# Kernel tuning notes

Hardware: AMD Instinct MI355X
Metric: run time of the kernel (lower is better)

The kernel has to match this reference:

```python
import jax, jax.numpy as jnp
from jax import lax
import numpy as np

B = 512
EPS = 1e-5


def _conv(x, w, b):
    # x: [B,C,H,W], w: [O,I,3,3], stride 1, pad 1 (same spatial)
    y = lax.conv_general_dilated(x, w, window_strides=(1, 1),
                                 padding=[(1, 1), (1, 1)],
                                 dimension_numbers=('NCHW', 'OIHW', 'NCHW'))
    return y + b[None, :, None, None]


def _bn(x, g, b, m, v):
    # eval-mode batchnorm with running stats
    inv = g * lax.rsqrt(v + EPS)
    return x * inv[None, :, None, None] + (b - m * inv)[None, :, None, None]


def _maxpool2(x):
    return lax.reduce_window(x, -jnp.inf, lax.max, (1, 1, 2, 2), (1, 1, 2, 2), 'VALID')


def _block(x, w, b, g, be, m, v):
    return _maxpool2(jax.nn.relu(_bn(_conv(x, w, b), g, be, m, v)))


def setup_inputs() -> dict:
    key = jax.random.key(0)
    ks = jax.random.split(key, 12)
    n = lambda k, s: jax.random.normal(k, s, jnp.float32) * 0.05
    z = lambda s: jnp.zeros(s, jnp.float32)
    o = lambda s: jnp.ones(s, jnp.float32)
    return {
        'x': jax.random.normal(ks[0], (B, 1, 48, 48), jnp.float32),
        'conv1_w': n(ks[1], (256, 1, 3, 3)), 'conv1_b': z((256,)),
        'bn1_g': o((256,)), 'bn1_b': z((256,)), 'bn1_m': z((256,)), 'bn1_v': o((256,)),
        'conv2_w': n(ks[2], (128, 256, 3, 3)), 'conv2_b': z((128,)),
        'bn2_g': o((128,)), 'bn2_b': z((128,)), 'bn2_m': z((128,)), 'bn2_v': o((128,)),
        'conv3_w': n(ks[3], (64, 128, 3, 3)), 'conv3_b': z((64,)),
        'bn3_g': o((64,)), 'bn3_b': z((64,)), 'bn3_m': z((64,)), 'bn3_v': o((64,)),
        'fc1_w': n(ks[4], (512, 2304)), 'fc1_b': z((512,)),
        'fc2_w': n(ks[5], (256, 512)), 'fc2_b': z((256,)),
        'att_w': n(ks[6], (64, 256)), 'att_b': z((64,)),
        'fc3_w': n(ks[7], (7, 64)), 'fc3_b': z((7,)),
    }


def reference(x, conv1_w, conv1_b, bn1_g, bn1_b, bn1_m, bn1_v,
              conv2_w, conv2_b, bn2_g, bn2_b, bn2_m, bn2_v,
              conv3_w, conv3_b, bn3_g, bn3_b, bn3_m, bn3_v,
              fc1_w, fc1_b, fc2_w, fc2_b, att_w, att_b, fc3_w, fc3_b):
    out1 = _block(x, conv1_w, conv1_b, bn1_g, bn1_b, bn1_m, bn1_v)      # [B,256,24,24]
    out2 = _block(out1, conv2_w, conv2_b, bn2_g, bn2_b, bn2_m, bn2_v)   # [B,128,12,12]
    out3 = _block(out2, conv3_w, conv3_b, bn3_g, bn3_b, bn3_m, bn3_v)   # [B,64,6,6]
    b_ = out3.shape[0]
    out4 = out3.reshape(b_, -1)                                          # [B,2304]
    out5 = out4 @ fc1_w.T + fc1_b                                        # [B,512]
    out6 = out5 @ fc2_w.T + fc2_b                                        # [B,256]
    # spatial attention: query projected to channel dim of out3
    q = out6 @ att_w.T + att_b                                           # [B,64]
    scores = jnp.einsum('bchw,bc->bhw', out3, q).reshape(b_, -1)         # [B,36]
    attn = jax.nn.softmax(scores, axis=1).reshape(b_, 6, 6)
    g_mod = jnp.einsum('bchw,bhw->bc', out3, attn)                       # [B,64]
    return g_mod @ fc3_w.T + fc3_b                                       # [B,7]
```

## Files before the change

### kernel.cpp

```cpp
#include <hip/hip_runtime.h>
#include <hip/hip_bf16.h>
#include <math.h>

#define EPS_BN 1e-5f

typedef __bf16 bf16x8 __attribute__((ext_vector_type(8)));
typedef float f32x4 __attribute__((ext_vector_type(4)));
typedef float f32x2 __attribute__((ext_vector_type(2)));

__device__ __forceinline__ void gl2lds16(const void* g, void* l) {
  __builtin_amdgcn_global_load_lds(
      (const __attribute__((address_space(1))) unsigned int*)g,
      (__attribute__((address_space(3))) unsigned int*)l, 16, 0, 0);
}

__global__ __launch_bounds__(256) void k_conv1(
    const float* __restrict__ x, const float* __restrict__ w,
    const float* __restrict__ cb, const float* __restrict__ g,
    const float* __restrict__ bb, const float* __restrict__ m,
    const float* __restrict__ v, __hip_bfloat16* __restrict__ out1p,
    __hip_bfloat16* __restrict__ out2p, const float* __restrict__ W32,
    const float* __restrict__ fc1w, float* __restrict__ Wet, int n1) {
  __shared__ float xp[14 * 50];
  const int bq = blockIdx.x;
  const int t = threadIdx.x;
  if (bq >= n1) {
    int idx = (bq - n1) * 256 + t;
    int r = idx / 2304, c = idx - r * 2304;
    float s = 0.f;
    for (int k = 0; k < 512; k++)
      s = fmaf(W32[r * 512 + k], fc1w[k * 2304 + c], s);
    Wet[c * 64 + r] = s;
    return;
  }
  const int b = bq >> 2, q = bq & 3;
  __hip_bfloat16* ob = out1p + (size_t)b * (26 * 26 * 256);
  const __hip_bfloat16 z = __float2bfloat16(0.f);
  if (q == 0)
    for (int i = t; i < 26 * 256; i += 256) ob[i] = z;
  if (q == 3)
    for (int i = t; i < 26 * 256; i += 256) ob[25 * 26 * 256 + i] = z;
  for (int i = t; i < 6 * 2 * 256; i += 256) {
    int r = 1 + 6 * q + (i >> 9), side = (i >> 8) & 1, c = i & 255;
    ob[(r * 26 + side * 25) * 256 + c] = z;
  }
  {
    __hip_bfloat16* o2 = out2p + (size_t)b * (14 * 14 * 128);
    if (q == 0)
      for (int i = t; i < 14 * 128; i += 256) o2[i] = z;
    if (q == 1)
      for (int i = t; i < 14 * 128; i += 256) o2[13 * 14 * 128 + i] = z;
    if (q == 2)
      for (int i = t; i < 6 * 2 * 128; i += 256) {
        int r = 1 + (i >> 8), side = (i >> 7) & 1, c = i & 127;
        o2[(r * 14 + side * 13) * 128 + c] = z;
      }
    if (q == 3)
      for (int i = t; i < 6 * 2 * 128; i += 256) {
        int r = 7 + (i >> 8), side = (i >> 7) & 1, c = i & 127;
        o2[(r * 14 + side * 13) * 128 + c] = z;
      }
  }
  for (int i = t; i < 14 * 50; i += 256) xp[i] = 0.f;
  __syncthreads();
  const float* xb = x + (size_t)b * 2304;
  for (int i = t; i < 14 * 48; i += 256) {
    int rr = i / 48, c = i - rr * 48;
    int gr = 12 * q - 1 + rr;
    if (gr >= 0 && gr < 48) xp[rr * 50 + c + 1] = xb[gr * 48 + c];
  }
  __syncthreads();
  float wr[9];
#pragma unroll
  for (int i = 0; i < 9; i++) wr[i] = w[t * 9 + i];
  const float scale = g[t] * rsqrtf(v[t] + EPS_BN);
  const float bias = (cb[t] - m[t]) * scale + bb[t];
#pragma unroll
  for (int ohl = 0; ohl < 6; ohl++) {
    const int r0 = 2 * ohl;
    f32x2 c01[4];
#pragma unroll
    for (int r = 0; r < 4; r++) c01[r] = *(const f32x2*)&xp[(r0 + r) * 50];
#pragma unroll 4
    for (int ow = 0; ow < 24; ow++) {
      f32x2 c23[4];
#pragma unroll
      for (int r = 0; r < 4; r++)
        c23[r] = *(const f32x2*)&xp[(r0 + r) * 50 + 2 * ow + 2];
      f32x2 s2a = 0.f, s2b = 0.f;
#pragma unroll
      for (int r = 0; r < 4; r++) {
        f32x2 p0 = c01[r], p2 = c23[r];
        f32x2 p1 = {p0.y, p2.x};
        if (r <= 2) {
          s2a += p0 * wr[r * 3 + 0];
          s2a += p1 * wr[r * 3 + 1];
          s2a += p2 * wr[r * 3 + 2];
        }
        if (r >= 1) {
          s2b += p0 * wr[(r - 1) * 3 + 0];
          s2b += p1 * wr[(r - 1) * 3 + 1];
          s2b += p2 * wr[(r - 1) * 3 + 2];
        }
      }
      f32x2 b0 = s2a * scale + bias;
      f32x2 b1 = s2b * scale + bias;
      float mx = fmaxf(fmaxf(b0.x, b0.y), fmaxf(b1.x, b1.y));
      ob[((6 * q + ohl + 1) * 26 + (ow + 1)) * 256 + t] =
          __float2bfloat16(fmaxf(mx, 0.f));
#pragma unroll
      for (int r = 0; r < 4; r++) c01[r] = c23[r];
    }
  }
}

__global__ void k_prep(const float* __restrict__ c2w,
                       __hip_bfloat16* __restrict__ wt2,
                       const float* __restrict__ c3w,
                       __hip_bfloat16* __restrict__ wt3,
                       const float* __restrict__ attw,
                       const float* __restrict__ fc2w, float* __restrict__ W32,
                       const float* __restrict__ fc1b,
                       const float* __restrict__ fc2b,
                       const float* __restrict__ attb, float* __restrict__ be) {
  const int blk = blockIdx.x, tid = threadIdx.x;
  if (blk < 1152) {
    int idx = blk * 256 + tid;
    int icr = idx & 7;
    int lhi = (idx >> 3) & 3;
    int oc = (idx >> 5) & 127;
    int rest = idx >> 12;
    int kb = rest & 7;
    int p = rest >> 3;
    int ic = kb * 32 + lhi * 8 + icr;
    wt2[idx] = __float2bfloat16(c2w[(oc * 256 + ic) * 9 + p]);
  } else if (blk < 1440) {
    int idx = (blk - 1152) * 256 + tid;
    int icr = idx & 7;
    int oc = (idx >> 3) & 63;
    int rest = idx >> 9;
    int icg = rest & 15;
    int p = rest >> 4;
    wt3[idx] = __float2bfloat16(c3w[(oc * 128 + icg * 8 + icr) * 9 + p]);
  } else if (blk < 1568) {
    int idx = (blk - 1440) * 256 + tid;
    int r = idx >> 9, c = idx & 511;
    float s = 0.f;
    for (int k = 0; k < 256; k++)
      s = fmaf(attw[r * 256 + k], fc2w[k * 512 + c], s);
    W32[idx] = s;
  } else {
    __shared__ float t1[256];
    float s = fc2b[tid];
    for (int k = 0; k < 512; k++) s = fmaf(fc2w[tid * 512 + k], fc1b[k], s);
    t1[tid] = s;
    __syncthreads();
    if (tid < 64) {
      float r = attb[tid];
      for (int k = 0; k < 256; k++) r = fmaf(attw[tid * 256 + k], t1[k], r);
      be[tid] = r;
    }
  }
}

__global__ __launch_bounds__(256) void k_mconv2(
    const __hip_bfloat16* __restrict__ in, const __hip_bfloat16* __restrict__ wt,
    const float* __restrict__ cb, const float* __restrict__ gg,
    const float* __restrict__ bbv, const float* __restrict__ bm,
    const float* __restrict__ bv, __hip_bfloat16* __restrict__ outp) {
  constexpr int HW = 24, IC = 256, OC = 128, HP = 26, CP = 26;
  constexpr int MTW = 6;
  constexpr int ROWS = 4;
  constexpr int TILES = 6;
  constexpr int WN = 32;
  constexpr int NF = 2;
  constexpr int NCH = 6 * CP * 8;
  constexpr int NCHP = (NCH + 255) & ~255;
  constexpr int NLD = NCHP / 256;
  constexpr int NSTG = 4;
  constexpr int ABUF = NCHP * 16;
  constexpr int KG = IC / 32;
  constexpr int EPITCH = OC + 1;
  constexpr int EBYTES = 48 * EPITCH * 4;
  constexpr int SMB = (2 * ABUF) > EBYTES ? (2 * ABUF) : EBYTES;
  constexpr int NSTEP = NSTG * 18;
  constexpr int D = 3;
  constexpr int AD = 3;

  __shared__ __align__(16) char smraw[SMB];
  float* se = (float*)smraw;

  const int tid = threadIdx.x;
  const int wn = tid >> 6, ln = tid & 63;
  const int lhi = ln >> 4, llo = ln & 15;

  const int per = gridDim.x >> 3;
  const int xcd = blockIdx.x & 7, sl = blockIdx.x >> 3;
  const int b = xcd * (per / TILES) + sl / TILES;
  const int T = sl % TILES;
  const int h0 = T * ROWS;

  const __hip_bfloat16* inb = in + (size_t)b * HP * HP * IC;

  int srcoff[NLD];
#pragma unroll
  for (int i = 0; i < NLD; i++) {
    int ci = tid + i * 256;
    if (ci >= NCH) ci = NCH - 1;
    int kgslot = ci & 7;
    int rest = ci >> 3;
    int c = rest % CP;
    int r = rest / CP;
    int kg = kgslot ^ (c & 7);
    srcoff[i] = ((h0 + r) * HP + c) * IC + kg * 8;
  }
  int abase9[3][3];
#pragma unroll
  for (int mt = 0; mt < 3; mt++) {
    int m = mt * 16 + llo;
    int hl = m / HW, wl = m % HW;
    int spb_ = (hl * CP + wl) * 8;
#pragma unroll
    for (int pw = 0; pw < 3; pw++)
      abase9[mt][pw] = (spb_ + pw * 8 + (lhi ^ ((wl + pw) & 7))) * 16;
  }
  const __hip_bfloat16* wtb = wt + (wn * WN + llo) * 32 + lhi * 8;

  f32x4 acc[MTW][NF];
  const f32x4 fz = {0.f, 0.f, 0.f, 0.f};
#pragma unroll
  for (int i = 0; i < MTW; i++)
#pragma unroll
    for (int j = 0; j < NF; j++) acc[i][j] = fz;

  auto LDA = [&](int s, int t, bf16x8* dst) {
    const int p = t >> 1, ks = t & 1;
    const int ph = p / 3, pw = p % 3;
    const int boff = ph * 3328 + ((s & 1) ? ABUF : 0);
#pragma unroll
    for (int mt = 0; mt < MTW; mt++) {
      int ab = abase9[mt % 3][pw];
      if (ks) ab ^= 64;
      dst[mt] = *(const bf16x8*)(smraw + ab + boff + (mt >= 3 ? 6656 : 0));
    }
  };

#pragma unroll
  for (int i = 0; i < NLD; i++)
    gl2lds16(inb + srcoff[i], smraw + (tid + i * 256) * 16);
  bf16x8 bq[D][NF];
#pragma unroll
  for (int d = 0; d < D; d++) {
    const int sg = d / 18, pg = (d % 18) >> 1, kf = d & 1;
#pragma unroll
    for (int j = 0; j < NF; j++)
      bq[d][j] = *(const bf16x8*)(wtb +
                                  (size_t)((pg * KG + sg * 2 + kf) * OC) * 32 +
                                  j * 512);
  }
  __syncthreads();

#pragma unroll
  for (int s = 0; s < NSTG; s++) {
    bf16x8 aq[AD][MTW];
    LDA(s, 0, aq[0]);
    LDA(s, 1, aq[1]);
#pragma unroll
    for (int t = 0; t < 18; t++) {
      const int g = s * 18 + t;
      if (t + 2 < 18) LDA(s, t + 2, aq[(t + 2) % AD]);
      __builtin_amdgcn_s_setprio(1);
#pragma unroll
      for (int mt = 0; mt < MTW; mt++)
#pragma unroll
        for (int j = 0; j < NF; j++)
          acc[mt][j] = __builtin_amdgcn_mfma_f32_16x16x32_bf16(
              aq[t % AD][mt], bq[g % D][j], acc[mt][j], 0, 0, 0);
      __builtin_amdgcn_s_setprio(0);
      if (g + D < NSTEP) {
        const int gf = g + D;
        const int sg = gf / 18, pg = (gf % 18) >> 1, kf = gf & 1;
#pragma unroll
        for (int j = 0; j < NF; j++)
          bq[gf % D][j] =
              *(const bf16x8*)(wtb +
                               (size_t)((pg * KG + sg * 2 + kf) * OC) * 32 +
                               j * 512);
      }
      if (t == 13 && s + 1 < NSTG) {
        char* nb = smraw + ((s + 1) & 1) * ABUF;
#pragma unroll
        for (int i = 0; i < NLD; i++)
          gl2lds16(inb + srcoff[i] + (s + 1) * 64, nb + (tid + i * 256) * 16);
      }
    }
    __syncthreads();
  }

  constexpr int OHW = HW / 2;
  constexpr int NP = 1 * OHW * OC;
#pragma unroll
  for (int pz = 0; pz < 2; pz++) {
    if (pz) __syncthreads();
#pragma unroll
    for (int j = 0; j < NF; j++) {
      int n = wn * WN + j * 16 + llo;
      float scale = gg[n] * rsqrtf(bv[n] + EPS_BN);
      float bias = (cb[n] - bm[n]) * scale + bbv[n];
#pragma unroll
      for (int mtl = 0; mtl < 3; mtl++)
#pragma unroll
        for (int r = 0; r < 4; r++) {
          int mrow = mtl * 16 + lhi * 4 + r;
          se[mrow * EPITCH + n] =
              fmaxf(acc[pz * 3 + mtl][j][r] * scale + bias, 0.f);
        }
    }
    __syncthreads();
    for (int sI = tid; sI < NP; sI += 256) {
      int n = sI % OC;
      int ow = (sI / OC) % OHW;
      int mloc = 2 * ow;
      float x0 = se[mloc * EPITCH + n];
      float x1 = se[(mloc + 1) * EPITCH + n];
      float x2 = se[(mloc + HW) * EPITCH + n];
      float x3 = se[(mloc + HW + 1) * EPITCH + n];
      float mx = fmaxf(fmaxf(x0, x1), fmaxf(x2, x3));
      int oh = (h0 >> 1) + pz;
      outp[(((size_t)b * 14 + oh + 1) * 14 + ow + 1) * OC + n] =
          __float2bfloat16(mx);
    }
  }
}

__global__ __launch_bounds__(256) void k_c3attn(
    const __hip_bfloat16* __restrict__ in, const __hip_bfloat16* __restrict__ wt,
    const float* __restrict__ cb, const float* __restrict__ gg,
    const float* __restrict__ bbv, const float* __restrict__ bm,
    const float* __restrict__ bv, const float* __restrict__ Wet,
    const float* __restrict__ be, const float* __restrict__ w3,
    const float* __restrict__ b3, float* __restrict__ out, int b0) {
  constexpr int HW = 12, IC = 128, OC = 64, HP = 14, CP = 14;
  constexpr int NCH = 14 * CP * 8;
  constexpr int NCHP = (NCH + 255) & ~255;
  constexpr int NLD = NCHP / 256;
  constexpr int NSTG = 2;
  constexpr int ABUF = NCHP * 16;
  constexpr int ICG = 16;
  constexpr int EPITCH = OC + 1;

  __shared__ __align__(16) char smraw[2 * ABUF];
  __shared__ float act[64 * 37];
  __shared__ float qp[4][64];
  __shared__ float ql[64], gm[64], sc[36];
  float* se = (float*)smraw;

  const int tid = threadIdx.x;
  const int wv = tid >> 6, ln = tid & 63;
  const int lhi = ln >> 4, llo = ln & 15;
  const int b = blockIdx.x;

  const __hip_bfloat16* inb = in + (size_t)b * HP * HP * IC;

  int srcoff[NLD];
#pragma unroll
  for (int i = 0; i < NLD; i++) {
    int ci = tid + i * 256;
    if (ci >= NCH) ci = NCH - 1;
    int kgslot = ci & 7;
    int rest = ci >> 3;
    int c = rest % CP;
    int r = rest / CP;
    int kg = kgslot ^ (c & 7);
    srcoff[i] = (r * HP + c) * IC + kg * 8;
  }
  int spb[9], wlv[9];
#pragma unroll
  for (int mt = 0; mt < 9; mt++) {
    int m = mt * 16 + llo;
    int hl = m / HW, wl = m % HW;
    spb[mt] = (hl * CP + wl) * 8;
    wlv[mt] = wl;
  }
  const __hip_bfloat16* wtb = wt + (size_t)(lhi * OC + wv * 16 + llo) * 8;

  f32x4 acc[9];
  const f32x4 fz = {0.f, 0.f, 0.f, 0.f};
#pragma unroll
  for (int i = 0; i < 9; i++) acc[i] = fz;

#pragma unroll
  for (int i = 0; i < NLD; i++)
    gl2lds16(inb + srcoff[i], smraw + (tid + i * 256) * 16);
  __syncthreads();

#pragma unroll
  for (int s = 0; s < NSTG; s++) {
    if (s + 1 < NSTG) {
      char* nb = smraw + ((s + 1) & 1) * ABUF;
#pragma unroll
      for (int i = 0; i < NLD; i++)
        gl2lds16(inb + srcoff[i] + (s + 1) * 64, nb + (tid + i * 256) * 16);
    }
    const char* cw = smraw + (s & 1) * ABUF;
#pragma unroll
    for (int tt = 0; tt < 18; tt++) {
      const int p = tt >> 1, ks = tt & 1;
      const int ph = p / 3, pw = p % 3;
      const int kg = ks * 4 + lhi;
      bf16x8 bf =
          *(const bf16x8*)(wtb + ((size_t)(p * ICG + s * 8 + ks * 4) * OC) * 8);
#pragma unroll
      for (int mt = 0; mt < 9; mt++) {
        int slot = spb[mt] + (ph * CP + pw) * 8 + (kg ^ ((wlv[mt] + pw) & 7));
        bf16x8 af = *(const bf16x8*)(cw + slot * 16);
        acc[mt] = __builtin_amdgcn_mfma_f32_16x16x32_bf16(af, bf, acc[mt], 0,
                                                          0, 0);
      }
    }
    __syncthreads();
  }

  {
    const int n = wv * 16 + llo;
    const float scale = gg[n] * rsqrtf(bv[n] + EPS_BN);
    const float bias = (cb[n] - bm[n]) * scale + bbv[n];
#pragma unroll
    for (int pz = 0; pz < 3; pz++) {
      if (pz) __syncthreads();
#pragma unroll
      for (int mtl = 0; mtl < 3; mtl++)
#pragma unroll
        for (int r = 0; r < 4; r++) {
          int mrow = mtl * 16 + lhi * 4 + r;
          se[mrow * EPITCH + n] =
              fmaxf(acc[pz * 3 + mtl][r] * scale + bias, 0.f);
        }
      __syncthreads();
      for (int sI = tid; sI < 2 * 6 * 64; sI += 256) {
        int nn = sI % 64;
        int ow = (sI / 64) % 6;
        int ohl = sI / (64 * 6);
        int mloc = (2 * ohl) * HW + 2 * ow;
        float x0 = se[mloc * EPITCH + nn];
        float x1 = se[(mloc + 1) * EPITCH + nn];
        float x2 = se[(mloc + HW) * EPITCH + nn];
        float x3 = se[(mloc + HW + 1) * EPITCH + nn];
        float mx = fmaxf(fmaxf(x0, x1), fmaxf(x2, x3));
        act[nn * 37 + (pz * 2 + ohl) * 6 + ow] = mx;
      }
    }
  }
  __syncthreads();

  {
    float qpv = 0.f;
    const int n = ln;
#pragma unroll 2
    for (int c2 = wv * 16; c2 < wv * 16 + 16; c2++)
      for (int hw = 0; hw < 36; hw++)
        qpv = fmaf(act[c2 * 37 + hw], Wet[(c2 * 36 + hw) * 64 + n], qpv);
    qp[wv][n] = qpv;
  }
  __syncthreads();
  if (tid < 64)
    ql[tid] = be[tid] + qp[0][tid] + qp[1][tid] + qp[2][tid] + qp[3][tid];
  __syncthreads();
  if (wv == 0) {
    float s = -INFINITY;
    if (ln < 36) {
      float a = 0.f;
      for (int c = 0; c < 64; c++) a = fmaf(act[c * 37 + ln], ql[c], a);
      s = a;
    }
    float mx = s;
    for (int off = 32; off >= 1; off >>= 1)
      mx = fmaxf(mx, __shfl_xor(mx, off));
    float e = (ln < 36) ? expf(s - mx) : 0.f;
    float sum = e;
    for (int off = 32; off >= 1; off >>= 1) sum += __shfl_xor(sum, off);
    if (ln < 36) sc[ln] = e / sum;
  }
  __syncthreads();
  if (wv == 0) {
    float gv = 0.f;
    for (int hw = 0; hw < 36; hw++) gv = fmaf(act[ln * 37 + hw], sc[hw], gv);
    gm[ln] = gv;
  }
  __syncthreads();
  if (tid < 7) {
    float a = b3[tid];
    for (int c = 0; c < 64; c++) a = fmaf(w3[tid * 64 + c], gm[c], a);
    out[(size_t)(b0 + b) * 7 + tid] = a;
  }
}

extern "C" void kernel_launch(void* const* d_in, const int* in_sizes, int n_in,
                              void* d_out, int out_size, void* d_ws,
                              size_t ws_size, hipStream_t stream) {
  const float* x    = (const float*)d_in[0];
  const float* c1w  = (const float*)d_in[1];
  const float* c1b  = (const float*)d_in[2];
  const float* g1   = (const float*)d_in[3];
  const float* bb1  = (const float*)d_in[4];
  const float* m1   = (const float*)d_in[5];
  const float* v1   = (const float*)d_in[6];
  const float* c2w  = (const float*)d_in[7];
  const float* c2b  = (const float*)d_in[8];
  const float* g2   = (const float*)d_in[9];
  const float* bb2  = (const float*)d_in[10];
  const float* m2   = (const float*)d_in[11];
  const float* v2   = (const float*)d_in[12];
  const float* c3w  = (const float*)d_in[13];
  const float* c3b  = (const float*)d_in[14];
  const float* g3   = (const float*)d_in[15];
  const float* bb3  = (const float*)d_in[16];
  const float* m3   = (const float*)d_in[17];
  const float* v3   = (const float*)d_in[18];
  const float* fc1w = (const float*)d_in[19];
  const float* fc1b = (const float*)d_in[20];
  const float* fc2w = (const float*)d_in[21];
  const float* fc2b = (const float*)d_in[22];
  const float* attw = (const float*)d_in[23];
  const float* attb = (const float*)d_in[24];
  const float* fc3w = (const float*)d_in[25];
  const float* fc3b = (const float*)d_in[26];

  const size_t PER_CHUNK = (173056ULL + 25088ULL) * 2;
  const size_t PERSIST = 589824 + 147456 + 131072 + 589824 + 256 + 8192;
  int CH = 512;
  while (CH > 8 && (size_t)CH * PER_CHUNK + PERSIST > ws_size) CH >>= 1;
  const int NCHK = 512 / CH;

  char* base = (char*)d_ws;
  size_t off = 0;
  auto alloc = [&](size_t nbytes) -> void* {
    void* p = base + off;
    off = (off + nbytes + 255) & ~(size_t)255;
    return p;
  };
  __hip_bfloat16* out1p = (__hip_bfloat16*)alloc((size_t)CH * 173056 * 2);
  __hip_bfloat16* out2p = (__hip_bfloat16*)alloc((size_t)CH * 25088 * 2);
  __hip_bfloat16* wt2  = (__hip_bfloat16*)alloc(589824);
  __hip_bfloat16* wt3  = (__hip_bfloat16*)alloc(147456);
  float* W32           = (float*)alloc(131072);
  float* Wet           = (float*)alloc(589824);
  float* be            = (float*)alloc(256);

  k_prep<<<1569, 256, 0, stream>>>(c2w, wt2, c3w, wt3, attw, fc2w, W32, fc1b,
                                   fc2b, attb, be);

  for (int c = 0; c < NCHK; c++) {
    const float* xc = x + (size_t)c * CH * 2304;
    const int n1 = CH * 4;
    const int grid1 = n1 + (c == 0 ? 576 : 0);
    k_conv1<<<grid1, 256, 0, stream>>>(xc, c1w, c1b, g1, bb1, m1, v1, out1p,
                                       out2p, W32, fc1w, Wet, n1);
    k_mconv2<<<CH * 6, 256, 0, stream>>>(out1p, wt2, c2b, g2, bb2, m2, v2,
                                         out2p);
    k_c3attn<<<CH, 256, 0, stream>>>(out2p, wt3, c3b, g3, bb3, m3, v3, Wet, be,
                                     fc3w, fc3b, (float*)d_out, c * CH);
  }
}
```

Baseline: 403.1 us.

## Fold weight prep into conv1 launch and move Wet folding into conv2 grid

Removes the standalone prep kernel launch by giving its blocks to the first-chunk conv1 grid, and moves the fc1-folding (Wet) blocks from the conv1 launch to extra blocks in the conv2 launch. Each weight transform now runs alongside independent work in the kernel that precedes its consumer, cutting one launch and a serialized dependency. It also precomputes both XOR-swizzled LDS base offsets per k-step, trading a few registers for fewer per-load ALU ops. One risk is that the extra tail blocks in conv2 could lengthen that kernel or change occupancy.

```diff
diff --git a/kernel.cpp b/kernel.cpp
--- a/kernel.cpp
+++ b/kernel.cpp
@@ -14,25 +14,61 @@
       (__attribute__((address_space(3))) unsigned int*)l, 16, 0, 0);
 }
 
-__global__ __launch_bounds__(256) void k_conv1(
+__global__ __launch_bounds__(256) void k_conv1prep(
     const float* __restrict__ x, const float* __restrict__ w,
     const float* __restrict__ cb, const float* __restrict__ g,
     const float* __restrict__ bb, const float* __restrict__ m,
     const float* __restrict__ v, __hip_bfloat16* __restrict__ out1p,
-    __hip_bfloat16* __restrict__ out2p, const float* __restrict__ W32,
-    const float* __restrict__ fc1w, float* __restrict__ Wet, int n1) {
+    __hip_bfloat16* __restrict__ out2p, const float* __restrict__ c2w,
+    __hip_bfloat16* __restrict__ wt2, const float* __restrict__ c3w,
+    __hip_bfloat16* __restrict__ wt3, const float* __restrict__ attw,
+    const float* __restrict__ fc2w, float* __restrict__ W32,
+    const float* __restrict__ fc1b, const float* __restrict__ fc2b,
+    const float* __restrict__ attb, float* __restrict__ be, int nprep) {
   __shared__ float xp[14 * 50];
-  const int bq = blockIdx.x;
+  const int blk = blockIdx.x;
   const int t = threadIdx.x;
-  if (bq >= n1) {
-    int idx = (bq - n1) * 256 + t;
-    int r = idx / 2304, c = idx - r * 2304;
-    float s = 0.f;
-    for (int k = 0; k < 512; k++)
-      s = fmaf(W32[r * 512 + k], fc1w[k * 2304 + c], s);
-    Wet[c * 64 + r] = s;
+  if (blk < nprep) {
+    if (blk < 1152) {
+      int idx = blk * 256 + t;
+      int icr = idx & 7;
+      int lhi = (idx >> 3) & 3;
+      int oc = (idx >> 5) & 127;
+      int rest = idx >> 12;
+      int kb = rest & 7;
+      int p = rest >> 3;
+      int ic = kb * 32 + lhi * 8 + icr;
+      wt2[idx] = __float2bfloat16(c2w[(oc * 256 + ic) * 9 + p]);
+    } else if (blk < 1440) {
+      int idx = (blk - 1152) * 256 + t;
+      int icr = idx & 7;
+      int oc = (idx >> 3) & 63;
+      int rest = idx >> 9;
+      int icg = rest & 15;
+      int p = rest >> 4;
+      wt3[idx] = __float2bfloat16(c3w[(oc * 128 + icg * 8 + icr) * 9 + p]);
+    } else if (blk < 1568) {
+      int idx = (blk - 1440) * 256 + t;
+      int r = idx >> 9, c = idx & 511;
+      float s = 0.f;
+      for (int k = 0; k < 256; k++)
+        s = fmaf(attw[r * 256 + k], fc2w[k * 512 + c], s);
+      W32[idx] = s;
+    } else {
+      float* t1 = xp;
+      float s = fc2b[t];
+      for (int k = 0; k < 512; k++) s = fmaf(fc2w[t * 512 + k], fc1b[k], s);
+      t1[t] = s;
+      __syncthreads();
+      if (t < 64) {
+        float r = attb[t];
+        for (int k = 0; k < 256; k++) r = fmaf(attw[t * 256 + k], t1[k], r);
+        be[t] = r;
+      }
+    }
     return;
   }
+  const int bq = blk - nprep;
   const int b = bq >> 2, q = bq & 3;
   __hip_bfloat16* ob = out1p + (size_t)b * (26 * 26 * 256);
   const __hip_bfloat16 z = __float2bfloat16(0.f);
@@ -114,60 +150,13 @@
   }
 }
 
-__global__ void k_prep(const float* __restrict__ c2w,
-                       __hip_bfloat16* __restrict__ wt2,
-                       const float* __restrict__ c3w,
-                       __hip_bfloat16* __restrict__ wt3,
-                       const float* __restrict__ attw,
-                       const float* __restrict__ fc2w, float* __restrict__ W32,
-                       const float* __restrict__ fc1b,
-                       const float* __restrict__ fc2b,
-                       const float* __restrict__ attb, float* __restrict__ be) {
-  const int blk = blockIdx.x, tid = threadIdx.x;
-  if (blk < 1152) {
-    int idx = blk * 256 + tid;
-    int icr = idx & 7;
-    int lhi = (idx >> 3) & 3;
-    int oc = (idx >> 5) & 127;
-    int rest = idx >> 12;
-    int kb = rest & 7;
-    int p = rest >> 3;
-    int ic = kb * 32 + lhi * 8 + icr;
-    wt2[idx] = __float2bfloat16(c2w[(oc * 256 + ic) * 9 + p]);
-  } else if (blk < 1440) {
-    int idx = (blk - 1152) * 256 + tid;
-    int icr = idx & 7;
-    int oc = (idx >> 3) & 63;
-    int rest = idx >> 9;
-    int icg = rest & 15;
-    int p = rest >> 4;
-    wt3[idx] = __float2bfloat16(c3w[(oc * 128 + icg * 8 + icr) * 9 + p]);
-  } else if (blk < 1568) {
-    int idx = (blk - 1440) * 256 + tid;
-    int r = idx >> 9, c = idx & 511;
-    float s = 0.f;
-    for (int k = 0; k < 256; k++)
-      s = fmaf(attw[r * 256 + k], fc2w[k * 512 + c], s);
-    W32[idx] = s;
-  } else {
-    __shared__ float t1[256];
-    float s = fc2b[tid];
-    for (int k = 0; k < 512; k++) s = fmaf(fc2w[tid * 512 + k], fc1b[k], s);
-    t1[tid] = s;
-    __syncthreads();
-    if (tid < 64) {
-      float r = attb[tid];
-      for (int k = 0; k < 256; k++) r = fmaf(attw[tid * 256 + k], t1[k], r);
-      be[tid] = r;
-    }
-  }
-}
-
 __global__ __launch_bounds__(256) void k_mconv2(
     const __hip_bfloat16* __restrict__ in, const __hip_bfloat16* __restrict__ wt,
     const float* __restrict__ cb, const float* __restrict__ gg,
     const float* __restrict__ bbv, const float* __restrict__ bm,
-    const float* __restrict__ bv, __hip_bfloat16* __restrict__ outp) {
+    const float* __restrict__ bv, __hip_bfloat16* __restrict__ outp,
+    const float* __restrict__ W32, const float* __restrict__ fc1w,
+    float* __restrict__ Wet, int n2) {
   constexpr int HW = 24, IC = 256, OC = 128, HP = 26, CP = 26;
   constexpr int MTW = 6;
   constexpr int ROWS = 4;
@@ -187,14 +176,24 @@
   constexpr int D = 3;
   constexpr int AD = 3;
 
+  const int tid = threadIdx.x;
+  if ((int)blockIdx.x >= n2) {
+    int idx = ((int)blockIdx.x - n2) * 256 + tid;
+    int r = idx / 2304, c = idx - r * 2304;
+    float s = 0.f;
+    for (int k = 0; k < 512; k++)
+      s = fmaf(W32[r * 512 + k], fc1w[k * 2304 + c], s);
+    Wet[c * 64 + r] = s;
+    return;
+  }
+
   __shared__ __align__(16) char smraw[SMB];
   float* se = (float*)smraw;
 
-  const int tid = threadIdx.x;
   const int wn = tid >> 6, ln = tid & 63;
   const int lhi = ln >> 4, llo = ln & 15;
 
-  const int per = gridDim.x >> 3;
+  const int per = n2 >> 3;
   const int xcd = blockIdx.x & 7, sl = blockIdx.x >> 3;
   const int b = xcd * (per / TILES) + sl / TILES;
   const int T = sl % TILES;
@@ -214,15 +213,18 @@
     int kg = kgslot ^ (c & 7);
     srcoff[i] = ((h0 + r) * HP + c) * IC + kg * 8;
   }
-  int abase9[3][3];
+  int abase[2][3][3];
 #pragma unroll
   for (int mt = 0; mt < 3; mt++) {
     int m = mt * 16 + llo;
     int hl = m / HW, wl = m % HW;
     int spb_ = (hl * CP + wl) * 8;
 #pragma unroll
-    for (int pw = 0; pw < 3; pw++)
-      abase9[mt][pw] = (spb_ + pw * 8 + (lhi ^ ((wl + pw) & 7))) * 16;
+    for (int pw = 0; pw < 3; pw++) {
+      int a0 = (spb_ + pw * 8 + (lhi ^ ((wl + pw) & 7))) * 16;
+      abase[0][mt][pw] = a0;
+      abase[1][mt][pw] = a0 ^ 64;
+    }
   }
   const __hip_bfloat16* wtb = wt + (wn * WN + llo) * 32 + lhi * 8;
 
@@ -239,9 +241,8 @@
     const int boff = ph * 3328 + ((s & 1) ? ABUF : 0);
 #pragma unroll
     for (int mt = 0; mt < MTW; mt++) {
-      int ab = abase9[mt % 3][pw];
-      if (ks) ab ^= 64;
-      dst[mt] = *(const bf16x8*)(smraw + ab + boff + (mt >= 3 ? 6656 : 0));
+      dst[mt] = *(const bf16x8*)(smraw + abase[ks][mt % 3][pw] + boff +
+                                 (mt >= 3 ? 6656 : 0));
     }
   };
 
@@ -547,17 +548,16 @@
   float* Wet           = (float*)alloc(589824);
   float* be            = (float*)alloc(256);
 
-  k_prep<<<1569, 256, 0, stream>>>(c2w, wt2, c3w, wt3, attw, fc2w, W32, fc1b,
-                                   fc2b, attb, be);
-
   for (int c = 0; c < NCHK; c++) {
     const float* xc = x + (size_t)c * CH * 2304;
-    const int n1 = CH * 4;
-    const int grid1 = n1 + (c == 0 ? 576 : 0);
-    k_conv1<<<grid1, 256, 0, stream>>>(xc, c1w, c1b, g1, bb1, m1, v1, out1p,
-                                       out2p, W32, fc1w, Wet, n1);
-    k_mconv2<<<CH * 6, 256, 0, stream>>>(out1p, wt2, c2b, g2, bb2, m2, v2,
-                                         out2p);
+    const int nprep = (c == 0) ? 1569 : 0;
+    k_conv1prep<<<nprep + CH * 4, 256, 0, stream>>>(
+        xc, c1w, c1b, g1, bb1, m1, v1, out1p, out2p, c2w, wt2, c3w, wt3, attw,
+        fc2w, W32, fc1b, fc2b, attb, be, nprep);
+    const int n2 = CH * 6;
+    const int grid2 = n2 + (c == 0 ? 576 : 0);
+    k_mconv2<<<grid2, 256, 0, stream>>>(out1p, wt2, c2b, g2, bb2, m2, v2,
+                                        out2p, W32, fc1w, Wet, n2);
     k_c3attn<<<CH, 256, 0, stream>>>(out2p, wt3, c3b, g3, bb3, m3, v3, Wet, be,
                                      fc3w, fc3b, (float*)d_out, c * CH);
   }
```

After: 404.6 us. About the same (+0.4%).
